# Kernel tuning notes

Measured on AMD Instinct MI355X. Metric: run time of the kernel, lower is better.

## Reference

```python
import jax, jax.numpy as jnp
import numpy as np

SHAPELET_SIZE = 64
NUM_SHAPELETS = 128
IN_CHANNELS = 8


def setup_inputs() -> dict:
    key = jax.random.key(0)
    k1, k2 = jax.random.split(key)
    x = jax.random.normal(k1, (64, IN_CHANNELS, 2048), dtype=jnp.float32)
    shapelets = jax.random.normal(k2, (IN_CHANNELS, NUM_SHAPELETS, SHAPELET_SIZE), dtype=jnp.float32)
    return {"x": x, "shapelets": shapelets}


def _znorm(s):
    # Z-normalize along the time-step axis (dim 2), matching Znormalize_dim(shapelets, 2)
    mu = jnp.mean(s, axis=2, keepdims=True)
    sd = jnp.std(s, axis=2, keepdims=True)
    return (s - mu) / sd


def reference(x, shapelets):
    # x: (N, C, L); shapelets: (C, K, S)
    S = shapelets.shape[-1]
    N, C, L = x.shape
    W = L - S + 1
    # unfold(2, S, 1): sliding windows -> (N, C, W, S)
    idx = jnp.arange(W)[:, None] + jnp.arange(S)[None, :]  # (W, S)
    xw = x[:, :, idx]  # (N, C, W, S)
    sh = _znorm(shapelets)  # (C, K, S)
    # Euclidean cdist via ||a||^2 + ||b||^2 - 2 a.b (avoids (N,C,W,K,S) blowup)
    sq_x = jnp.sum(xw * xw, axis=-1)          # (N, C, W)
    sq_s = jnp.sum(sh * sh, axis=-1)          # (C, K)
    cross = jnp.einsum('ncws,cks->ncwk', xw, sh)  # (N, C, W, K)
    d2 = sq_x[..., None] + sq_s[None, :, None, :] - 2.0 * cross
    d = jnp.sqrt(jnp.maximum(d2, 1e-12))      # (N, C, W, K)
    # sum over channels, then global min over windows -> (N, 1, K)
    dsum = jnp.sum(d, axis=1)                 # (N, W, K)
    out = jnp.min(dsum, axis=1)[:, None, :]   # (N, 1, K)
    return out
```

## Files before the change

kernel.cpp:

```cpp
#include <hip/hip_runtime.h>
#include <hip/hip_bf16.h>
#include <math.h>

#define C 8
#define K 128
#define S 64
#define L 2048
#define NB 64
#define W (L - S + 1)
#define TW 128
#define NTW 16
#define XCS 208
#define XFS 200

typedef __attribute__((ext_vector_type(8))) short bf16x8;
typedef __attribute__((ext_vector_type(4))) float f32x4;

__device__ __forceinline__ unsigned short f2bf(float f) {
  unsigned int u = __float_as_uint(f);
  u += 0x7FFFu + ((u >> 16) & 1u);
  return (unsigned short)(u >> 16);
}

__device__ __forceinline__ unsigned int pkbf(float a, float b) {
  __hip_bfloat162 h = __float22bfloat162_rn(make_float2(a, b));
  return *reinterpret_cast<unsigned int*>(&h);
}

__device__ __forceinline__ void gll16(const void* g, void* l) {
  __builtin_amdgcn_global_load_lds((const __attribute__((address_space(1))) void*)g,
                                   (__attribute__((address_space(3))) void*)l, 16, 0, 0);
}

__global__ __launch_bounds__(256) void prep_kernel(const float* __restrict__ sh,
                                                   unsigned short* __restrict__ shzB,
                                                   float* __restrict__ out) {
  int tid = blockIdx.x * 256 + threadIdx.x;
  if (tid < NB * K) out[tid] = __int_as_float(0x7F800000);
  int gid = blockIdx.x * 4 + (threadIdx.x >> 6);
  int lane = threadIdx.x & 63;
  float v = sh[(size_t)gid * S + lane];
  float s1 = v, s2 = v * v;
#pragma unroll
  for (int off = 32; off > 0; off >>= 1) {
    s1 += __shfl_down(s1, off);
    s2 += __shfl_down(s2, off);
  }
  s1 = __shfl(s1, 0);
  s2 = __shfl(s2, 0);
  float mu = s1 * (1.0f / S);
  float sd = sqrtf(fmaxf(s2 * (1.0f / S) - mu * mu, 0.0f));
  float z = (v - mu) / sd;
  int c = gid >> 7, k = gid & (K - 1), s = lane;
  int idx = c * 8192 + (k >> 6) * 4096 + ((((k >> 4) & 3) * 2) + (s >> 5)) * 512 +
            ((((s >> 3) & 3) * 16 + (k & 15)) * 8) + (s & 7);
  shzB[idx] = f2bf(-2.0f * z);
}

__global__ __launch_bounds__(256, 2) void main_kernel(const float* __restrict__ x,
                                                      const unsigned short* __restrict__ shzB,
                                                      int* __restrict__ out) {
  __shared__ __align__(16) unsigned short bbuf[2][8192];
  __shared__ __align__(16) unsigned short xcop[C][8][XCS];
  __shared__ __align__(16) float sqx[C][TW];

  const int t = threadIdx.x;
  const int lane = t & 63;
  const int wave = t >> 6;
  const int wgrp = wave & 1;
  const int kgrp = wave >> 1;
  const int col = lane & 15;
  const int quad = lane >> 4;
  const int n = blockIdx.y;
  const int w0 = blockIdx.x * TW;
  const float* xn = x + (size_t)n * C * L;
  const unsigned short* bsrc = shzB;

  float* xf = (float*)bbuf;
#pragma unroll
  for (int cc = 0; cc < 2; ++cc) {
    const int c = wave * 2 + cc;
    const int e = lane * 4;
    float4 v; v.x = v.y = v.z = v.w = 0.0f;
    if (lane < 48) {
      int g = w0 + e;
      if (g + 3 < L) {
        v = *(const float4*)(xn + c * L + g);
      } else {
        v.x = (g + 0 < L) ? xn[c * L + g + 0] : 0.0f;
        v.y = (g + 1 < L) ? xn[c * L + g + 1] : 0.0f;
        v.z = (g + 2 < L) ? xn[c * L + g + 2] : 0.0f;
        v.w = (g + 3 < L) ? xn[c * L + g + 3] : 0.0f;
      }
    }
    if (lane < 50) *(float4*)&xf[c * XFS + e] = v;
  }
  __syncthreads();

#pragma unroll
  for (int cc = 0; cc < 2; ++cc) {
    const int cb = wave * 2 + cc;
    const int rb = lane >> 3;
    const int c8 = lane & 7;
    const float* xr = xf + cb * XFS;
#pragma unroll
    for (int j = 0; j < 12; ++j) {
      int i = (c8 + j * 8) * 2;
      *(unsigned int*)&xcop[cb][rb][i] = pkbf(xr[i + rb], xr[i + rb + 1]);
    }
  }
#pragma unroll
  for (int cc = 0; cc < 2; ++cc) {
    const int c = wave * 2 + cc, wl = lane * 2;
    const float* xr = xf + c * XFS;
    float p0 = 0.f, p1 = 0.f, p2 = 0.f, p3 = 0.f;
#pragma unroll
    for (int si = 0; si < S; si += 4) {
      float v0 = xr[wl + si], v1 = xr[wl + si + 1], v2 = xr[wl + si + 2], v3 = xr[wl + si + 3];
      p0 = fmaf(v0, v0, p0); p1 = fmaf(v1, v1, p1);
      p2 = fmaf(v2, v2, p2); p3 = fmaf(v3, v3, p3);
    }
    float s0 = 64.0f + (p0 + p1) + (p2 + p3);
    sqx[c][wl] = s0;
    float a = xr[wl + S], b = xr[wl];
    sqx[c][wl + 1] = s0 + a * a - b * b;
  }
  __syncthreads();

#pragma unroll
  for (int i = 0; i < 4; ++i)
    gll16(bsrc + i * 2048 + t * 8, &bbuf[0][i * 2048 + wave * 512]);

  const f32x4 z4 = {0.0f, 0.0f, 0.0f, 0.0f};
  f32x4 dsum[4][4];
#pragma unroll
  for (int kt = 0; kt < 4; ++kt)
#pragma unroll
    for (int wt = 0; wt < 4; ++wt) dsum[kt][wt] = z4;

  const int r8 = col & 7;
  const int abase = wgrp * 64 + (col - r8) + quad * 8;

  for (int c = 0; c < C; ++c) {
    __syncthreads();

    if (c + 1 < C) {
#pragma unroll
      for (int i = 0; i < 4; ++i)
        gll16(bsrc + (c + 1) * 8192 + i * 2048 + t * 8,
              &bbuf[(c + 1) & 1][i * 2048 + wave * 512]);
    }

    const unsigned short* bb = &bbuf[c & 1][kgrp * 4096];
    bf16x8 b00 = *(const bf16x8*)(bb + 0 * 512 + lane * 8);
    bf16x8 b01 = *(const bf16x8*)(bb + 1 * 512 + lane * 8);
    bf16x8 b10 = *(const bf16x8*)(bb + 2 * 512 + lane * 8);
    bf16x8 b11 = *(const bf16x8*)(bb + 3 * 512 + lane * 8);
    bf16x8 b20 = *(const bf16x8*)(bb + 4 * 512 + lane * 8);
    bf16x8 b21 = *(const bf16x8*)(bb + 5 * 512 + lane * 8);
    bf16x8 b30 = *(const bf16x8*)(bb + 6 * 512 + lane * 8);
    bf16x8 b31 = *(const bf16x8*)(bb + 7 * 512 + lane * 8);

    const unsigned short* xc = &xcop[c][r8][0];
#pragma unroll
    for (int wt = 0; wt < 4; ++wt) {
      f32x4 ai = *(const f32x4*)&sqx[c][wgrp * 64 + wt * 16 + quad * 4];
      bf16x8 x0 = *(const bf16x8*)(xc + abase + wt * 16);
      bf16x8 x1 = *(const bf16x8*)(xc + abase + wt * 16 + 32);
      f32x4 a0 = __builtin_amdgcn_mfma_f32_16x16x32_bf16(x0, b00, ai, 0, 0, 0);
      f32x4 a1 = __builtin_amdgcn_mfma_f32_16x16x32_bf16(x0, b10, ai, 0, 0, 0);
      f32x4 a2 = __builtin_amdgcn_mfma_f32_16x16x32_bf16(x0, b20, ai, 0, 0, 0);
      f32x4 a3 = __builtin_amdgcn_mfma_f32_16x16x32_bf16(x0, b30, ai, 0, 0, 0);
      a0 = __builtin_amdgcn_mfma_f32_16x16x32_bf16(x1, b01, a0, 0, 0, 0);
      a1 = __builtin_amdgcn_mfma_f32_16x16x32_bf16(x1, b11, a1, 0, 0, 0);
      a2 = __builtin_amdgcn_mfma_f32_16x16x32_bf16(x1, b21, a2, 0, 0, 0);
      a3 = __builtin_amdgcn_mfma_f32_16x16x32_bf16(x1, b31, a3, 0, 0, 0);
#pragma unroll
      for (int i = 0; i < 4; ++i) {
        dsum[0][wt][i] += __builtin_amdgcn_sqrtf(fmaxf(a0[i], 0.0f));
        dsum[1][wt][i] += __builtin_amdgcn_sqrtf(fmaxf(a1[i], 0.0f));
        dsum[2][wt][i] += __builtin_amdgcn_sqrtf(fmaxf(a2[i], 0.0f));
        dsum[3][wt][i] += __builtin_amdgcn_sqrtf(fmaxf(a3[i], 0.0f));
      }
    }
  }

  const float INF = __int_as_float(0x7F800000);
  const int wbase = w0 + wgrp * 64;
#pragma unroll
  for (int kt = 0; kt < 4; ++kt) {
    float mv = INF;
#pragma unroll
    for (int wt = 0; wt < 4; ++wt)
#pragma unroll
      for (int i = 0; i < 4; ++i) {
        int w = wbase + wt * 16 + quad * 4 + i;
        mv = (w < W) ? fminf(mv, dsum[kt][wt][i]) : mv;
      }
    mv = fminf(mv, __shfl_xor(mv, 16));
    mv = fminf(mv, __shfl_xor(mv, 32));
    if (quad == 0)
      atomicMin(&out[n * K + kgrp * 64 + kt * 16 + col], __float_as_int(mv));
  }
}

extern "C" void kernel_launch(void* const* d_in, const int* in_sizes, int n_in,
                              void* d_out, int out_size, void* d_ws, size_t ws_size,
                              hipStream_t stream) {
  const float* x = (const float*)d_in[0];
  const float* sh = (const float*)d_in[1];
  float* out = (float*)d_out;
  unsigned short* shzB = (unsigned short*)d_ws;

  prep_kernel<<<256, 256, 0, stream>>>(sh, shzB, out);
  main_kernel<<<dim3(NTW, NB), 256, 0, stream>>>(x, shzB, (int*)out);
}
```

Measured before the change: 92.28 us.

## Load shapelet B fragments directly into registers instead of LDS double-buffer

Drops the LDS double buffer for the shapelet operand and the per-channel barrier. Each wave now loads its B fragments straight from global memory into a register double buffer, prefetching the next channel while computing the current one. LDS use shrinks (x staging gets its own small array), and launch bounds ask for 3 blocks per CU to raise occupancy. The cost is more VGPRs (16 bf16x8 vectors) and possible spills under the tighter register budget, and global-load latency may be exposed without an LDS stage.

```diff
diff --git a/kernel.cpp b/kernel.cpp
--- a/kernel.cpp
+++ b/kernel.cpp
@@ -27,11 +27,6 @@
   return *reinterpret_cast<unsigned int*>(&h);
 }
 
-__device__ __forceinline__ void gll16(const void* g, void* l) {
-  __builtin_amdgcn_global_load_lds((const __attribute__((address_space(1))) void*)g,
-                                   (__attribute__((address_space(3))) void*)l, 16, 0, 0);
-}
-
 __global__ __launch_bounds__(256) void prep_kernel(const float* __restrict__ sh,
                                                    unsigned short* __restrict__ shzB,
                                                    float* __restrict__ out) {
@@ -57,12 +52,12 @@
   shzB[idx] = f2bf(-2.0f * z);
 }
 
-__global__ __launch_bounds__(256, 2) void main_kernel(const float* __restrict__ x,
+__global__ __launch_bounds__(256, 3) void main_kernel(const float* __restrict__ x,
                                                       const unsigned short* __restrict__ shzB,
                                                       int* __restrict__ out) {
-  __shared__ __align__(16) unsigned short bbuf[2][8192];
   __shared__ __align__(16) unsigned short xcop[C][8][XCS];
   __shared__ __align__(16) float sqx[C][TW];
+  __shared__ __align__(16) float xf[C][XFS];
 
   const int t = threadIdx.x;
   const int lane = t & 63;
@@ -74,9 +69,14 @@
   const int n = blockIdx.y;
   const int w0 = blockIdx.x * TW;
   const float* xn = x + (size_t)n * C * L;
-  const unsigned short* bsrc = shzB;
-
-  float* xf = (float*)bbuf;
+  const unsigned short* bw = shzB + kgrp * 4096 + lane * 8;
+
+  bf16x8 B[2][8];
+#pragma unroll
+  for (int i = 0; i < 8; ++i)
+    B[0][i] = *(const bf16x8*)(bw + i * 512);
+
+  float* xfp = &xf[0][0];
 #pragma unroll
   for (int cc = 0; cc < 2; ++cc) {
     const int c = wave * 2 + cc;
@@ -93,7 +93,7 @@
         v.w = (g + 3 < L) ? xn[c * L + g + 3] : 0.0f;
       }
     }
-    if (lane < 50) *(float4*)&xf[c * XFS + e] = v;
+    if (lane < 50) *(float4*)&xfp[c * XFS + e] = v;
   }
   __syncthreads();
 
@@ -102,7 +102,7 @@
     const int cb = wave * 2 + cc;
     const int rb = lane >> 3;
     const int c8 = lane & 7;
-    const float* xr = xf + cb * XFS;
+    const float* xr = xfp + cb * XFS;
 #pragma unroll
     for (int j = 0; j < 12; ++j) {
       int i = (c8 + j * 8) * 2;
@@ -112,7 +112,7 @@
 #pragma unroll
   for (int cc = 0; cc < 2; ++cc) {
     const int c = wave * 2 + cc, wl = lane * 2;
-    const float* xr = xf + c * XFS;
+    const float* xr = xfp + c * XFS;
     float p0 = 0.f, p1 = 0.f, p2 = 0.f, p3 = 0.f;
 #pragma unroll
     for (int si = 0; si < S; si += 4) {
@@ -127,10 +127,6 @@
   }
   __syncthreads();
 
-#pragma unroll
-  for (int i = 0; i < 4; ++i)
-    gll16(bsrc + i * 2048 + t * 8, &bbuf[0][i * 2048 + wave * 512]);
-
   const f32x4 z4 = {0.0f, 0.0f, 0.0f, 0.0f};
   f32x4 dsum[4][4];
 #pragma unroll
@@ -141,25 +137,13 @@
   const int r8 = col & 7;
   const int abase = wgrp * 64 + (col - r8) + quad * 8;
 
+#pragma unroll
   for (int c = 0; c < C; ++c) {
-    __syncthreads();
-
     if (c + 1 < C) {
 #pragma unroll
-      for (int i = 0; i < 4; ++i)
-        gll16(bsrc + (c + 1) * 8192 + i * 2048 + t * 8,
-              &bbuf[(c + 1) & 1][i * 2048 + wave * 512]);
-    }
-
-    const unsigned short* bb = &bbuf[c & 1][kgrp * 4096];
-    bf16x8 b00 = *(const bf16x8*)(bb + 0 * 512 + lane * 8);
-    bf16x8 b01 = *(const bf16x8*)(bb + 1 * 512 + lane * 8);
-    bf16x8 b10 = *(const bf16x8*)(bb + 2 * 512 + lane * 8);
-    bf16x8 b11 = *(const bf16x8*)(bb + 3 * 512 + lane * 8);
-    bf16x8 b20 = *(const bf16x8*)(bb + 4 * 512 + lane * 8);
-    bf16x8 b21 = *(const bf16x8*)(bb + 5 * 512 + lane * 8);
-    bf16x8 b30 = *(const bf16x8*)(bb + 6 * 512 + lane * 8);
-    bf16x8 b31 = *(const bf16x8*)(bb + 7 * 512 + lane * 8);
+      for (int i = 0; i < 8; ++i)
+        B[(c + 1) & 1][i] = *(const bf16x8*)(bw + (c + 1) * 8192 + i * 512);
+    }
 
     const unsigned short* xc = &xcop[c][r8][0];
 #pragma unroll
@@ -167,14 +151,14 @@
       f32x4 ai = *(const f32x4*)&sqx[c][wgrp * 64 + wt * 16 + quad * 4];
       bf16x8 x0 = *(const bf16x8*)(xc + abase + wt * 16);
       bf16x8 x1 = *(const bf16x8*)(xc + abase + wt * 16 + 32);
-      f32x4 a0 = __builtin_amdgcn_mfma_f32_16x16x32_bf16(x0, b00, ai, 0, 0, 0);
-      f32x4 a1 = __builtin_amdgcn_mfma_f32_16x16x32_bf16(x0, b10, ai, 0, 0, 0);
-      f32x4 a2 = __builtin_amdgcn_mfma_f32_16x16x32_bf16(x0, b20, ai, 0, 0, 0);
-      f32x4 a3 = __builtin_amdgcn_mfma_f32_16x16x32_bf16(x0, b30, ai, 0, 0, 0);
-      a0 = __builtin_amdgcn_mfma_f32_16x16x32_bf16(x1, b01, a0, 0, 0, 0);
-      a1 = __builtin_amdgcn_mfma_f32_16x16x32_bf16(x1, b11, a1, 0, 0, 0);
-      a2 = __builtin_amdgcn_mfma_f32_16x16x32_bf16(x1, b21, a2, 0, 0, 0);
-      a3 = __builtin_amdgcn_mfma_f32_16x16x32_bf16(x1, b31, a3, 0, 0, 0);
+      f32x4 a0 = __builtin_amdgcn_mfma_f32_16x16x32_bf16(x0, B[c & 1][0], ai, 0, 0, 0);
+      f32x4 a1 = __builtin_amdgcn_mfma_f32_16x16x32_bf16(x0, B[c & 1][2], ai, 0, 0, 0);
+      f32x4 a2 = __builtin_amdgcn_mfma_f32_16x16x32_bf16(x0, B[c & 1][4], ai, 0, 0, 0);
+      f32x4 a3 = __builtin_amdgcn_mfma_f32_16x16x32_bf16(x0, B[c & 1][6], ai, 0, 0, 0);
+      a0 = __builtin_amdgcn_mfma_f32_16x16x32_bf16(x1, B[c & 1][1], a0, 0, 0, 0);
+      a1 = __builtin_amdgcn_mfma_f32_16x16x32_bf16(x1, B[c & 1][3], a1, 0, 0, 0);
+      a2 = __builtin_amdgcn_mfma_f32_16x16x32_bf16(x1, B[c & 1][5], a2, 0, 0, 0);
+      a3 = __builtin_amdgcn_mfma_f32_16x16x32_bf16(x1, B[c & 1][7], a3, 0, 0, 0);
 #pragma unroll
       for (int i = 0; i < 4; ++i) {
         dsum[0][wt][i] += __builtin_amdgcn_sqrtf(fmaxf(a0[i], 0.0f));
```

Result: slower. 262.6 us (+184.6%).
